# Kernel optimization log

Hardware: AMD Instinct MI355X
Metric: run time of the kernel (lower is better)

The kernel has to match this reference:

```python
import jax, jax.numpy as jnp
import numpy as np

NUM_CLASSES = 1000
FEAT_DIM = 256
MOMENTUM = 0.99
WARMUP_EPOCHS = 5
TEMPERATURE = 1.0
EPS = 1e-12  # torch F.normalize eps


def l2norm(x):
    # F.normalize(x, p=2, dim=-1): x / max(||x||, eps)
    n = jnp.linalg.norm(x, axis=-1, keepdims=True)
    return x / jnp.maximum(n, EPS)


def setup_inputs() -> dict:
    key = jax.random.key(0)
    k1, k2, k3 = jax.random.split(key, 3)
    features = jax.random.normal(k1, (131072, FEAT_DIM), dtype=jnp.float32)
    prototypes = jax.random.normal(k2, (NUM_CLASSES, FEAT_DIM), dtype=jnp.float32)
    labels = jax.random.randint(k3, (131072,), 0, NUM_CLASSES, dtype=jnp.int32)
    initialized = jnp.ones((NUM_CLASSES,), dtype=bool)
    return {"features": features, "prototypes": prototypes, "labels": labels,
            "initialized": initialized, "epoch": 10}


def reference(features, prototypes, labels, initialized, epoch):
    # ---- update(): vectorized per-class masked mean + momentum EMA ----
    momentum = 0.0 if (epoch is not None and epoch < WARMUP_EPOCHS) else MOMENTUM
    f = l2norm(features)                                   # [N, D]
    sums = jax.ops.segment_sum(f, labels, num_segments=NUM_CLASSES)        # [C, D]
    counts = jax.ops.segment_sum(jnp.ones((f.shape[0],), f.dtype), labels,
                                 num_segments=NUM_CLASSES)                 # [C]
    present = counts > 0                                    # classes with samples
    class_mean = l2norm(sums / jnp.maximum(counts, 1.0)[:, None])          # [C, D]
    if momentum == 0.0:
        cand = class_mean
    else:
        ema = l2norm(momentum * prototypes + (1.0 - momentum) * class_mean)
        cand = jnp.where(initialized[:, None], ema, class_mean)
    new_protos = jnp.where(present[:, None], cand, prototypes)             # [C, D]
    new_protos = jax.lax.stop_gradient(new_protos)  # update() is @torch.no_grad

    # ---- compute_logits(): normalize + cdist ----
    fn = l2norm(features)                                   # [N, D]
    pn = l2norm(new_protos)                                 # [C, D]
    sq = (jnp.sum(fn * fn, -1)[:, None] + jnp.sum(pn * pn, -1)[None, :]
          - 2.0 * fn @ pn.T)                                # [N, C]
    dist = jnp.sqrt(jnp.maximum(sq, 0.0))
    return -dist / TEMPERATURE
```

## Files before the change

kernel.cpp:

```cpp
#include <hip/hip_runtime.h>

typedef float f32x4 __attribute__((ext_vector_type(4)));
typedef __bf16 bf16x8 __attribute__((ext_vector_type(8)));
typedef unsigned short u16;

#define NUM_CLASSES 1000
#define CPAD 1024
#define FEAT 256
#define BUCKET_CAP 512

__device__ __forceinline__ u16 f2bf(float f) {
  unsigned u = __float_as_uint(f);
  u += 0x7fffu + ((u >> 16) & 1u);
  return (u16)(u >> 16);
}

__device__ __forceinline__ float wave_sum(float v) {
#pragma unroll
  for (int m = 1; m < 64; m <<= 1) v += __shfl_xor(v, m, 64);
  return v;
}

__device__ __forceinline__ void gload16(const void* g, void* l) {
  __builtin_amdgcn_global_load_lds(
      (const __attribute__((address_space(1))) void*)g,
      (__attribute__((address_space(3))) void*)l, 16, 0, 0);
}

__global__ __launch_bounds__(256) void knorm(
    const float* __restrict__ feats, const int* __restrict__ labels,
    u16* __restrict__ fnbf, int* __restrict__ cursor,
    int* __restrict__ bucket) {
  int row = blockIdx.x * 4 + (threadIdx.x >> 6);
  int lane = threadIdx.x & 63;
  const float4 v = *(const float4*)(feats + (size_t)row * FEAT + lane * 4);
  float ss = v.x * v.x + v.y * v.y + v.z * v.z + v.w * v.w;
  ss = wave_sum(ss);
  float r = 1.0f / fmaxf(sqrtf(ss), 1e-12f);
  ushort4 o = make_ushort4(f2bf(v.x * r), f2bf(v.y * r), f2bf(v.z * r),
                           f2bf(v.w * r));
  *(ushort4*)(fnbf + (size_t)row * FEAT + lane * 4) = o;
  if (lane == 0) {
    int lab = labels[row];
    int slot = atomicAdd(&cursor[lab], 1);
    if (slot < BUCKET_CAP) bucket[lab * BUCKET_CAP + slot] = row;
  }
}

__global__ __launch_bounds__(256) void kupdate(
    const float* __restrict__ protos, const int* __restrict__ inited,
    const int* __restrict__ epoch_p, const u16* __restrict__ fnbf,
    const int* __restrict__ bucket, const int* __restrict__ cursor,
    u16* __restrict__ pnbf, float* __restrict__ npn) {
  int c = blockIdx.x;
  int tid = threadIdx.x;
  int lane = tid & 63, w = tid >> 6;
  if (c >= NUM_CLASSES) {
    if (w == 0) *(ushort4*)(pnbf + (size_t)c * FEAT + lane * 4) =
        make_ushort4(0, 0, 0, 0);
    if (tid == 0) npn[c] = 0.0f;
    return;
  }
  int icnt = cursor[c];
  int gcnt = min(icnt, BUCKET_CAP);
  const int* blist = bucket + c * BUCKET_CAP;
  f32x4 accv = {0.f, 0.f, 0.f, 0.f};
  for (int rIt = w; rIt < gcnt; rIt += 4) {
    int row = blist[rIt];
    ushort4 u = *(const ushort4*)(fnbf + (size_t)row * FEAT + lane * 4);
    accv[0] += __uint_as_float((unsigned)u.x << 16);
    accv[1] += __uint_as_float((unsigned)u.y << 16);
    accv[2] += __uint_as_float((unsigned)u.z << 16);
    accv[3] += __uint_as_float((unsigned)u.w << 16);
  }
  __shared__ f32x4 smem[4][64];
  smem[w][lane] = accv;
  __syncthreads();
  if (w != 0) return;
  f32x4 s = smem[0][lane];
#pragma unroll
  for (int ww = 1; ww < 4; ww++) s += smem[ww][lane];

  float cnt = (float)icnt;
  const float4 p = *(const float4*)(protos + (size_t)c * FEAT + lane * 4);
  float ic = 1.0f / fmaxf(cnt, 1.0f);
  float mx = s[0] * ic, my = s[1] * ic, mz = s[2] * ic, mw = s[3] * ic;
  float ss = wave_sum(mx * mx + my * my + mz * mz + mw * mw);
  float r = 1.0f / fmaxf(sqrtf(ss), 1e-12f);
  mx *= r; my *= r; mz *= r; mw *= r;
  int epoch = *epoch_p;
  float mom = (epoch < 5) ? 0.0f : 0.99f;
  float cx, cy, cz, cw;
  if (mom == 0.0f) {
    cx = mx; cy = my; cz = mz; cw = mw;
  } else {
    float ex = mom * p.x + (1.0f - mom) * mx;
    float ey = mom * p.y + (1.0f - mom) * my;
    float ez = mom * p.z + (1.0f - mom) * mz;
    float ew = mom * p.w + (1.0f - mom) * mw;
    float ss2 = wave_sum(ex * ex + ey * ey + ez * ez + ew * ew);
    float r2 = 1.0f / fmaxf(sqrtf(ss2), 1e-12f);
    ex *= r2; ey *= r2; ez *= r2; ew *= r2;
    bool ini = inited[c] != 0;
    cx = ini ? ex : mx; cy = ini ? ey : my;
    cz = ini ? ez : mz; cw = ini ? ew : mw;
  }
  bool present = icnt > 0;
  float nx = present ? cx : p.x, ny = present ? cy : p.y;
  float nz = present ? cz : p.z, nw = present ? cw : p.w;
  float ss3 = wave_sum(nx * nx + ny * ny + nz * nz + nw * nw);
  float r3 = 1.0f / fmaxf(sqrtf(ss3), 1e-12f);
  nx *= r3; ny *= r3; nz *= r3; nw *= r3;
  if (lane == 0) npn[c] = ss3 * r3 * r3;
  *(ushort4*)(pnbf + (size_t)c * FEAT + lane * 4) =
      make_ushort4(f2bf(nx), f2bf(ny), f2bf(nz), f2bf(nw));
}

__global__ __launch_bounds__(512, 2) void kgemm(
    const u16* __restrict__ A, const u16* __restrict__ B,
    float* __restrict__ out) {
  __shared__ __align__(16) u16 S[32768];
  int bm = blockIdx.x;
  int tid = threadIdx.x;
  int lane = tid & 63, w = tid >> 6;
  char* Asb = (char*)S;
  char* Bw = (char*)S + 32768 + w * 4096;

  const char* Ag = (const char*)A + (size_t)bm * 64 * 512;

#pragma unroll
  for (int r = 0; r < 4; r++) {
    int row = r * 16 + w * 2 + (lane >> 5);
    int csw = ((lane & 31) ^ (row & 7)) << 4;
    gload16(Ag + (size_t)row * 512 + csw, Asb + r * 8192 + w * 1024);
  }

  int fr = lane & 15;
  int ks = lane >> 4;

#pragma unroll 1
  for (int bnp = 0; bnp < 2; bnp++) {
    const char* Bg = (const char*)B + ((size_t)bnp * 512 + w * 64) * 512;
#pragma unroll
    for (int j = 0; j < 4; j++) {
      int col = j * 16 + (lane >> 2);
      int ksw = ((lane & 3) ^ (col & 3)) << 4;
      gload16(Bg + (size_t)col * 512 + ksw, Bw + j * 1024);
    }
    asm volatile("s_waitcnt vmcnt(0)" ::: "memory");
    if (bnp == 0) __syncthreads();

    f32x4 acc[4][4];
#pragma unroll
    for (int m = 0; m < 4; m++)
#pragma unroll
      for (int n = 0; n < 4; n++) acc[m][n] = f32x4{0.f, 0.f, 0.f, 0.f};

#pragma unroll 1
    for (int t = 0; t < 8; t++) {
      bf16x8 av[4], bv[4];
#pragma unroll
      for (int m = 0; m < 4; m++)
        av[m] = *(const bf16x8*)(Asb + (m * 16 + fr) * 512 +
                                 (((t * 4 + ks) ^ (fr & 7)) << 4));
#pragma unroll
      for (int n = 0; n < 4; n++)
        bv[n] = *(const bf16x8*)(Bw + (n * 16 + fr) * 64 +
                                 ((ks ^ (fr & 3)) << 4));
      asm volatile("" ::"v"(av[0]), "v"(av[1]), "v"(av[2]), "v"(av[3]),
                   "v"(bv[0]), "v"(bv[1]), "v"(bv[2]), "v"(bv[3]));
      if (t < 7) {
#pragma unroll
        for (int j = 0; j < 4; j++) {
          int col = j * 16 + (lane >> 2);
          int ksw = ((lane & 3) ^ (col & 3)) << 4;
          gload16(Bg + (size_t)col * 512 + (t + 1) * 64 + ksw, Bw + j * 1024);
        }
      }
#pragma unroll
      for (int m = 0; m < 4; m++)
#pragma unroll
        for (int n = 0; n < 4; n++)
          acc[m][n] = __builtin_amdgcn_mfma_f32_16x16x32_bf16(
              av[m], bv[n], acc[m][n], 0, 0, 0);
      if (t < 7) asm volatile("s_waitcnt vmcnt(0)" ::: "memory");
    }

    int col0 = bnp * 512 + w * 64 + fr;
    int rbase = bm * 64 + (lane >> 4) * 4;
#pragma unroll
    for (int m = 0; m < 4; m++) {
      int row0 = rbase + m * 16;
#pragma unroll
      for (int n = 0; n < 4; n++) {
        int col = col0 + n * 16;
        if (col >= NUM_CLASSES) continue;
        float sq0 = 2.0f - 2.0f * acc[m][n][0];
        float sq1 = 2.0f - 2.0f * acc[m][n][1];
        float sq2 = 2.0f - 2.0f * acc[m][n][2];
        float sq3 = 2.0f - 2.0f * acc[m][n][3];
        float* o = out + (size_t)row0 * NUM_CLASSES + col;
        o[0] = -sqrtf(fmaxf(sq0, 0.0f));
        o[NUM_CLASSES] = -sqrtf(fmaxf(sq1, 0.0f));
        o[2 * NUM_CLASSES] = -sqrtf(fmaxf(sq2, 0.0f));
        o[3 * NUM_CLASSES] = -sqrtf(fmaxf(sq3, 0.0f));
      }
    }
  }
}

extern "C" void kernel_launch(void* const* d_in, const int* in_sizes, int n_in,
                              void* d_out, int out_size, void* d_ws,
                              size_t ws_size, hipStream_t stream) {
  const float* feats = (const float*)d_in[0];
  const float* protos = (const float*)d_in[1];
  const int* labels = (const int*)d_in[2];
  const int* inited = (const int*)d_in[3];
  const int* epoch_p = (const int*)d_in[4];
  float* out = (float*)d_out;
  int N = in_sizes[0] / FEAT;

  char* ws = (char*)d_ws;
  size_t off = 0;
  u16* fnbf = (u16*)(ws + off);    off += (size_t)N * FEAT * 2;
  int* cursor = (int*)(ws + off);  off += (size_t)CPAD * 4;
  int* bucket = (int*)(ws + off);  off += (size_t)CPAD * BUCKET_CAP * 4;
  u16* pnbf = (u16*)(ws + off);    off += (size_t)CPAD * FEAT * 2;
  float* npn = (float*)(ws + off); off += (size_t)CPAD * 4;
  (void)ws_size; (void)n_in; (void)out_size;

  hipMemsetAsync(cursor, 0, (size_t)CPAD * 4, stream);

  knorm<<<N / 4, 256, 0, stream>>>(feats, labels, fnbf, cursor, bucket);
  kupdate<<<CPAD, 256, 0, stream>>>(protos, inited, epoch_p, fnbf, bucket,
                                    cursor, pnbf, npn);
  kgemm<<<N / 64, 512, 0, stream>>>(fnbf, pnbf, out);
}
```

Before: 273.1 us.

## Overlap first column-half output stores with second-half MFMA loop in GEMM

The two column-half passes of the GEMM are unrolled into separate accumulator sets, and the epilogue stores for the first half are spread across the iterations of the second half's K loop. The intent is to hide the large output write traffic behind MFMA compute instead of running them serially. The wait in the second loop is relaxed to vmcnt(8) so pending stores do not stall the B-tile loads. The cost is a doubled accumulator register footprint, which may lower occupancy or cause spills under launch_bounds(512,2), and the vmcnt accounting depends on exact instruction counts.

After: 372.0 us. 36.2% more time.

```diff
diff --git a/kernel.cpp b/kernel.cpp
--- a/kernel.cpp
+++ b/kernel.cpp
@@ -138,73 +138,126 @@
   int fr = lane & 15;
   int ks = lane >> 4;
 
+  const char* Bg0 = (const char*)B + ((size_t)w * 64) * 512;
+#pragma unroll
+  for (int j = 0; j < 4; j++) {
+    int col = j * 16 + (lane >> 2);
+    int ksw = ((lane & 3) ^ (col & 3)) << 4;
+    gload16(Bg0 + (size_t)col * 512 + ksw, Bw + j * 1024);
+  }
+  asm volatile("s_waitcnt vmcnt(0)" ::: "memory");
+  __syncthreads();
+
+  f32x4 acc0[4][4];
+#pragma unroll
+  for (int m = 0; m < 4; m++)
+#pragma unroll
+    for (int n = 0; n < 4; n++) acc0[m][n] = f32x4{0.f, 0.f, 0.f, 0.f};
+
 #pragma unroll 1
-  for (int bnp = 0; bnp < 2; bnp++) {
-    const char* Bg = (const char*)B + ((size_t)bnp * 512 + w * 64) * 512;
-#pragma unroll
-    for (int j = 0; j < 4; j++) {
-      int col = j * 16 + (lane >> 2);
-      int ksw = ((lane & 3) ^ (col & 3)) << 4;
-      gload16(Bg + (size_t)col * 512 + ksw, Bw + j * 1024);
-    }
-    asm volatile("s_waitcnt vmcnt(0)" ::: "memory");
-    if (bnp == 0) __syncthreads();
-
-    f32x4 acc[4][4];
-#pragma unroll
-    for (int m = 0; m < 4; m++)
-#pragma unroll
-      for (int n = 0; n < 4; n++) acc[m][n] = f32x4{0.f, 0.f, 0.f, 0.f};
+  for (int t = 0; t < 8; t++) {
+    bf16x8 av[4], bv[4];
+#pragma unroll
+    for (int m = 0; m < 4; m++)
+      av[m] = *(const bf16x8*)(Asb + (m * 16 + fr) * 512 +
+                               (((t * 4 + ks) ^ (fr & 7)) << 4));
+#pragma unroll
+    for (int n = 0; n < 4; n++)
+      bv[n] = *(const bf16x8*)(Bw + (n * 16 + fr) * 64 +
+                               ((ks ^ (fr & 3)) << 4));
+    asm volatile("" ::"v"(av[0]), "v"(av[1]), "v"(av[2]), "v"(av[3]),
+                 "v"(bv[0]), "v"(bv[1]), "v"(bv[2]), "v"(bv[3]));
+    if (t < 7) {
+#pragma unroll
+      for (int j = 0; j < 4; j++) {
+        int col = j * 16 + (lane >> 2);
+        int ksw = ((lane & 3) ^ (col & 3)) << 4;
+        gload16(Bg0 + (size_t)col * 512 + (t + 1) * 64 + ksw, Bw + j * 1024);
+      }
+    }
+#pragma unroll
+    for (int m = 0; m < 4; m++)
+#pragma unroll
+      for (int n = 0; n < 4; n++)
+        acc0[m][n] = __builtin_amdgcn_mfma_f32_16x16x32_bf16(av[m], bv[n],
+                                                             acc0[m][n], 0, 0, 0);
+    if (t < 7) asm volatile("s_waitcnt vmcnt(0)" ::: "memory");
+  }
+
+  const char* Bg1 = (const char*)B + ((size_t)512 + w * 64) * 512;
+#pragma unroll
+  for (int j = 0; j < 4; j++) {
+    int col = j * 16 + (lane >> 2);
+    int ksw = ((lane & 3) ^ (col & 3)) << 4;
+    gload16(Bg1 + (size_t)col * 512 + ksw, Bw + j * 1024);
+  }
+  asm volatile("s_waitcnt vmcnt(0)" ::: "memory");
+
+  f32x4 acc1[4][4];
+#pragma unroll
+  for (int m = 0; m < 4; m++)
+#pragma unroll
+    for (int n = 0; n < 4; n++) acc1[m][n] = f32x4{0.f, 0.f, 0.f, 0.f};
+
+  int col0p0 = w * 64 + fr;
+  int rbase = bm * 64 + (lane >> 4) * 4;
 
 #pragma unroll 1
-    for (int t = 0; t < 8; t++) {
-      bf16x8 av[4], bv[4];
-#pragma unroll
-      for (int m = 0; m < 4; m++)
-        av[m] = *(const bf16x8*)(Asb + (m * 16 + fr) * 512 +
-                                 (((t * 4 + ks) ^ (fr & 7)) << 4));
+  for (int t = 0; t < 8; t++) {
+    if (t > 0) {
+      asm volatile("s_waitcnt vmcnt(8)" ::: "memory");
+      __builtin_amdgcn_sched_barrier(0);
+    }
+    bf16x8 av[4], bv[4];
+#pragma unroll
+    for (int m = 0; m < 4; m++)
+      av[m] = *(const bf16x8*)(Asb + (m * 16 + fr) * 512 +
+                               (((t * 4 + ks) ^ (fr & 7)) << 4));
+#pragma unroll
+    for (int n = 0; n < 4; n++)
+      bv[n] = *(const bf16x8*)(Bw + (n * 16 + fr) * 64 +
+                               ((ks ^ (fr & 3)) << 4));
+    asm volatile("" ::"v"(av[0]), "v"(av[1]), "v"(av[2]), "v"(av[3]),
+                 "v"(bv[0]), "v"(bv[1]), "v"(bv[2]), "v"(bv[3]));
+    if (t < 7) {
+#pragma unroll
+      for (int j = 0; j < 4; j++) {
+        int col = j * 16 + (lane >> 2);
+        int ksw = ((lane & 3) ^ (col & 3)) << 4;
+        gload16(Bg1 + (size_t)col * 512 + (t + 1) * 64 + ksw, Bw + j * 1024);
+      }
+    }
+#pragma unroll
+    for (int pi = 0; pi < 2; pi++) {
+      int p = 2 * t + pi;
+      int m = p >> 2, n = p & 3;
+      int row0 = rbase + m * 16;
+      float* o = out + (size_t)row0 * NUM_CLASSES + col0p0 + n * 16;
+      o[0] = -sqrtf(fmaxf(2.0f - 2.0f * acc0[m][n][0], 0.0f));
+      o[NUM_CLASSES] = -sqrtf(fmaxf(2.0f - 2.0f * acc0[m][n][1], 0.0f));
+      o[2 * NUM_CLASSES] = -sqrtf(fmaxf(2.0f - 2.0f * acc0[m][n][2], 0.0f));
+      o[3 * NUM_CLASSES] = -sqrtf(fmaxf(2.0f - 2.0f * acc0[m][n][3], 0.0f));
+    }
+#pragma unroll
+    for (int m = 0; m < 4; m++)
 #pragma unroll
       for (int n = 0; n < 4; n++)
-        bv[n] = *(const bf16x8*)(Bw + (n * 16 + fr) * 64 +
-                                 ((ks ^ (fr & 3)) << 4));
-      asm volatile("" ::"v"(av[0]), "v"(av[1]), "v"(av[2]), "v"(av[3]),
-                   "v"(bv[0]), "v"(bv[1]), "v"(bv[2]), "v"(bv[3]));
-      if (t < 7) {
-#pragma unroll
-        for (int j = 0; j < 4; j++) {
-          int col = j * 16 + (lane >> 2);
-          int ksw = ((lane & 3) ^ (col & 3)) << 4;
-          gload16(Bg + (size_t)col * 512 + (t + 1) * 64 + ksw, Bw + j * 1024);
-        }
-      }
-#pragma unroll
-      for (int m = 0; m < 4; m++)
-#pragma unroll
-        for (int n = 0; n < 4; n++)
-          acc[m][n] = __builtin_amdgcn_mfma_f32_16x16x32_bf16(
-              av[m], bv[n], acc[m][n], 0, 0, 0);
-      if (t < 7) asm volatile("s_waitcnt vmcnt(0)" ::: "memory");
-    }
-
-    int col0 = bnp * 512 + w * 64 + fr;
-    int rbase = bm * 64 + (lane >> 4) * 4;
-#pragma unroll
-    for (int m = 0; m < 4; m++) {
-      int row0 = rbase + m * 16;
-#pragma unroll
-      for (int n = 0; n < 4; n++) {
-        int col = col0 + n * 16;
-        if (col >= NUM_CLASSES) continue;
-        float sq0 = 2.0f - 2.0f * acc[m][n][0];
-        float sq1 = 2.0f - 2.0f * acc[m][n][1];
-        float sq2 = 2.0f - 2.0f * acc[m][n][2];
-        float sq3 = 2.0f - 2.0f * acc[m][n][3];
-        float* o = out + (size_t)row0 * NUM_CLASSES + col;
-        o[0] = -sqrtf(fmaxf(sq0, 0.0f));
-        o[NUM_CLASSES] = -sqrtf(fmaxf(sq1, 0.0f));
-        o[2 * NUM_CLASSES] = -sqrtf(fmaxf(sq2, 0.0f));
-        o[3 * NUM_CLASSES] = -sqrtf(fmaxf(sq3, 0.0f));
-      }
+        acc1[m][n] = __builtin_amdgcn_mfma_f32_16x16x32_bf16(av[m], bv[n],
+                                                             acc1[m][n], 0, 0, 0);
+  }
+
+#pragma unroll
+  for (int m = 0; m < 4; m++) {
+    int row0 = rbase + m * 16;
+#pragma unroll
+    for (int n = 0; n < 4; n++) {
+      int col = 512 + w * 64 + fr + n * 16;
+      if (col >= NUM_CLASSES) continue;
+      float* o = out + (size_t)row0 * NUM_CLASSES + col;
+      o[0] = -sqrtf(fmaxf(2.0f - 2.0f * acc1[m][n][0], 0.0f));
+      o[NUM_CLASSES] = -sqrtf(fmaxf(2.0f - 2.0f * acc1[m][n][1], 0.0f));
+      o[2 * NUM_CLASSES] = -sqrtf(fmaxf(2.0f - 2.0f * acc1[m][n][2], 0.0f));
+      o[3 * NUM_CLASSES] = -sqrtf(fmaxf(2.0f - 2.0f * acc1[m][n][3], 0.0f));
     }
   }
 }
```
